# Performance work log

Measured on AMD Instinct MI355X. Metric: run time of the kernel, lower is better.

The kernel has to match this reference:

```python
import jax, jax.numpy as jnp
from jax import lax
import numpy as np

# GConv2d config (matches init_kwargs)
OUT_TRANSFORMS = 4  # rotations: 0, 90, 180, 270 degrees
STRIDE = 1
PADDING = 1


def setup_inputs() -> dict:
    key = jax.random.key(0)
    k1, k2, k3, k4 = jax.random.split(key, 4)
    B, IC_EFF, H, W = 16, 256, 64, 64   # IC_EFF = in_channels * in_transformations
    OC, K, F = 64, 4, 3                 # out_channels, num_dynamic_kernels, filter_size
    x = jax.random.normal(k1, (B, IC_EFF, H, W), dtype=jnp.float32)
    W_fc = jax.random.normal(k2, (K, IC_EFF), dtype=jnp.float32) * (1.0 / np.sqrt(IC_EFF))
    b_fc = jnp.zeros((K,), dtype=jnp.float32)
    kernel_bank = jax.random.normal(k3, (K, OC, IC_EFF, F, F), dtype=jnp.float32)
    return {"x": x, "W_fc": W_fc, "b_fc": b_fc, "kernel_bank": kernel_bank}


def reference(x, W_fc, b_fc, kernel_bank):
    B, C, H, W = x.shape
    # Dynamic routing: global average pool -> linear -> softmax over kernel bank
    pooled = x.mean(axis=(2, 3))                      # [B, C]
    coeffs = jax.nn.softmax(pooled @ W_fc.T + b_fc, axis=1)  # [B, K]
    # Sample-specific base kernels: mix of kernel bank
    base = jnp.einsum('bk,kocij->bocij', coeffs, kernel_bank)  # [B, oc, C, f, f]
    # P4 orientation expansion: rotate kernel spatially, stack along out-channels
    oriented = jnp.concatenate(
        [jnp.rot90(base, k, axes=(-2, -1)) for k in range(OUT_TRANSFORMS)], axis=1
    )  # [B, 4*oc, C, f, f]
    O, f = oriented.shape[1], oriented.shape[-1]
    # Batched per-sample conv via grouped convolution (one launch instead of B)
    xg = x.reshape(1, B * C, H, W)
    kg = oriented.reshape(B * O, C, f, f)
    out = lax.conv_general_dilated(
        xg, kg,
        window_strides=(STRIDE, STRIDE),
        padding=[(PADDING, PADDING), (PADDING, PADDING)],
        dimension_numbers=('NCHW', 'OIHW', 'NCHW'),
        feature_group_count=B,
    )  # [1, B*O, H', W']
    Ho, Wo = out.shape[-2], out.shape[-1]
    return out.reshape(B, O, Ho, Wo)
```

## Files before the change

kernel.cpp:

```cpp
#include <hip/hip_runtime.h>

#define B_  16
#define C_  256
#define O_  256

typedef short    bf16x8 __attribute__((ext_vector_type(8)));
typedef float    f32x16 __attribute__((ext_vector_type(16)));
typedef unsigned u32x4  __attribute__((ext_vector_type(4)));

#define XROW_SH  1056
#define XBC_SH   (66 * XROW_SH)
#define XT_BYTES ((size_t)B_ * 16 * XBC_SH * 2)

#define WTILE_SH 9216
#define WORP_BYTES ((size_t)B_ * 16 * 4 * WTILE_SH * 2)

#define XBUF_SH  10752

__device__ __forceinline__ unsigned cvtpk(float lo, float hi) {
    unsigned r;
    asm("v_cvt_pk_bf16_f32 %0, %1, %2" : "=v"(r) : "v"(lo), "v"(hi));
    return r;
}

__device__ __forceinline__ void gload16(const void* g, void* l) {
    __builtin_amdgcn_global_load_lds(
        (const __attribute__((address_space(1))) unsigned int*)g,
        (__attribute__((address_space(3))) unsigned int*)l, 16, 0, 0);
}

__global__ __launch_bounds__(256) void xprep_kernel(const float* __restrict__ x,
                                                    short* __restrict__ xT,
                                                    float* __restrict__ pooled4) {
    const int cg = blockIdx.x;
    const int b  = blockIdx.y;
    const int z  = blockIdx.z;
    const int t  = threadIdx.x;
    const int lane = t & 63, wv = t >> 6;
    const int cc = cg >> 1, lh = cg & 1;

    short* xTb = xT + (size_t)(b * 16 + cc) * XBC_SH;
    const float* xb = x + ((size_t)(b * C_ + cg * 8) << 12);

    {
        u32x4 zv = {0, 0, 0, 0};
        if (t < 32) {
            int r   = z * 16 + 1 + (t >> 1);
            int col = (t & 1) ? 65 : 0;
            *(u32x4*)&xTb[r * XROW_SH + lh * 528 + col * 8] = zv;
        }
        if (z == 0 || z == 3) {
            int row = (z == 0) ? 0 : 65;
            if (t < 66) *(u32x4*)&xTb[row * XROW_SH + lh * 528 + t * 8] = zv;
        }
    }

    float s[8] = {0.f, 0.f, 0.f, 0.f, 0.f, 0.f, 0.f, 0.f};
    const int px = lane;
#pragma unroll
    for (int r = 0; r < 4; ++r) {
        const int row = z * 16 + wv * 4 + r;
        const float* src = xb + row * 64 + px;
        float v[8];
#pragma unroll
        for (int i = 0; i < 8; ++i) { v[i] = src[(size_t)i << 12]; s[i] += v[i]; }
        u32x4 d = { cvtpk(v[0], v[1]), cvtpk(v[2], v[3]),
                    cvtpk(v[4], v[5]), cvtpk(v[6], v[7]) };
        *(u32x4*)&xTb[(row + 1) * XROW_SH + lh * 528 + (px + 1) * 8] = d;
    }

#pragma unroll
    for (int i = 0; i < 8; ++i)
#pragma unroll
        for (int off = 32; off; off >>= 1) s[i] += __shfl_xor(s[i], off, 64);

    __shared__ float pr[4][8];
    if (lane == 0) {
#pragma unroll
        for (int i = 0; i < 8; ++i) pr[wv][i] = s[i];
    }
    __syncthreads();
    if (t < 8) {
        float v = pr[0][t] + pr[1][t] + pr[2][t] + pr[3][t];
        pooled4[(z * B_ + b) * C_ + cg * 8 + t] = v * (1.0f / 4096.0f);
    }
}

__global__ __launch_bounds__(256) void mix_kernel(const float* __restrict__ bank,
                                                  const float* __restrict__ pooled4,
                                                  const float* __restrict__ W_fc,
                                                  const float* __restrict__ b_fc,
                                                  short* __restrict__ worp) {
    const int cc = blockIdx.x;
    const int og = blockIdx.y;
    const int t  = threadIdx.x;

    __shared__ float bankL[4][4][16][10];
    __shared__ float pl[64][4];
    __shared__ float cfs[16][4];

    for (int i = t; i < 2304; i += 256) {
        int k  = i / 576, r = i % 576;
        int oc = r / 144, r2 = r % 144;
        int c  = r2 / 9,  tap = r2 % 9;
        bankL[k][oc][c][tap] =
            bank[(((size_t)k * 64 + og * 4 + oc) * C_ + cc * 16 + c) * 9 + tap];
    }
    {
        int pair = t >> 2, seg = t & 3;
        int b = pair >> 2, k = pair & 3;
        float s = 0.f;
        for (int ci = 0; ci < 64; ++ci) {
            int c = seg * 64 + ci;
            float pv = pooled4[b * C_ + c] + pooled4[(B_ + b) * C_ + c]
                     + pooled4[(2 * B_ + b) * C_ + c] + pooled4[(3 * B_ + b) * C_ + c];
            s += pv * W_fc[k * C_ + c];
        }
        pl[pair][seg] = s;
    }
    __syncthreads();
    if (t < 64) {
        int b = t >> 2, k = t & 3;
        cfs[b][k] = pl[t][0] + pl[t][1] + pl[t][2] + pl[t][3] + b_fc[k];
    }
    __syncthreads();
    if (t < 16) {
        float l0 = cfs[t][0], l1 = cfs[t][1], l2 = cfs[t][2], l3 = cfs[t][3];
        float mx = fmaxf(fmaxf(l0, l1), fmaxf(l2, l3));
        float e0 = expf(l0 - mx), e1 = expf(l1 - mx);
        float e2 = expf(l2 - mx), e3 = expf(l3 - mx);
        float inv = 1.f / (e0 + e1 + e2 + e3);
        cfs[t][0] = e0 * inv; cfs[t][1] = e1 * inv;
        cfs[t][2] = e2 * inv; cfs[t][3] = e3 * inv;
    }
    __syncthreads();

    const int oc_l = t & 3;
    const int lhs  = (t >> 2) & 1;
    const int b    = (t >> 3) & 15;
    const int rep  = t >> 7;
    const int o64  = og * 4 + oc_l;

    const float c0 = cfs[b][0], c1 = cfs[b][1], c2 = cfs[b][2], c3 = cfs[b][3];
    float mixed[8][9];
#pragma unroll
    for (int ci = 0; ci < 8; ++ci)
#pragma unroll
        for (int tp = 0; tp < 9; ++tp)
            mixed[ci][tp] = c0 * bankL[0][oc_l][lhs * 8 + ci][tp]
                          + c1 * bankL[1][oc_l][lhs * 8 + ci][tp]
                          + c2 * bankL[2][oc_l][lhs * 8 + ci][tp]
                          + c3 * bankL[3][oc_l][lhs * 8 + ci][tp];

#define STOREOQ(OQ)                                                             \
    _Pragma("unroll")                                                           \
    for (int td = 0; td < 9; ++td) {                                            \
        const int ti = td / 3, tj = td % 3;                                     \
        int si, sj;                                                             \
        if      ((OQ) == 0) { si = ti;     sj = tj;     }                       \
        else if ((OQ) == 1) { si = tj;     sj = 2 - ti; }                       \
        else if ((OQ) == 2) { si = 2 - ti; sj = 2 - tj; }                       \
        else                { si = 2 - tj; sj = ti;     }                       \
        const int ts = si * 3 + sj;                                             \
        u32x4 d = { cvtpk(mixed[0][ts], mixed[1][ts]),                          \
                    cvtpk(mixed[2][ts], mixed[3][ts]),                          \
                    cvtpk(mixed[4][ts], mixed[5][ts]),                          \
                    cvtpk(mixed[6][ts], mixed[7][ts]) };                        \
        size_t base = ((((((size_t)b * 16 + cc) * 4 + (OQ)) * 9 + td) * 2       \
                        + lhs) * 64 + o64) * 8;                                 \
        *(u32x4*)&worp[base] = d;                                               \
    }

    if (rep == 0) { STOREOQ(0) STOREOQ(1) }
    else          { STOREOQ(2) STOREOQ(3) }
#undef STOREOQ
}

__global__ __launch_bounds__(256, 2)
void conv_mfma(const short* __restrict__ xT, const short* __restrict__ worp,
               float* __restrict__ out) {
    __shared__ short lds[2 * XBUF_SH + 2 * WTILE_SH];

    const int g    = blockIdx.x;
    const int w    = (g & 7) * 64 + (g >> 3);
    const int oq   = w & 3;
    const int m    = w >> 2;
    const int rowt = m & 7;
    const int b    = m >> 3;
    const int y0   = rowt * 8;

    const int t    = threadIdx.x;
    const int lane = t & 63;
    const int wid  = t >> 6;
    const int l31  = lane & 31;
    const int lh   = lane >> 5;

    const char* xsrcB = (const char*)xT
        + ((size_t)(b * 16) * XBC_SH + (size_t)y0 * XROW_SH) * 2 + lane * 16;
    const char* wsrcB = (const char*)worp
        + (((size_t)(b * 16) * 4) + oq) * (WTILE_SH * 2) + lane * 16;

#define STAGE(ccc, p)                                                           \
    { const char* xs = xsrcB + (size_t)(ccc) * (XBC_SH * 2);                    \
      const char* ws = wsrcB + (size_t)(ccc) * (4 * WTILE_SH * 2);              \
      char* xd = (char*)lds + (p) * (XBUF_SH * 2);                              \
      char* wd = (char*)lds + 2 * (XBUF_SH * 2) + (p) * (WTILE_SH * 2);         \
      for (int u = wid; u < 21; u += 4) gload16(xs + u * 1024, xd + u * 1024);  \
      for (int u = wid; u < 18; u += 4) gload16(ws + u * 1024, wd + u * 1024); }

#define BRD(r, s) (*(const bf16x8*)&xcur[(((r) * 2 + lh) * 66 + (s) + l31) * 8])
#define LOADROW(R, r)                                                           \
    { R[0] = BRD(r, 0);  R[1] = BRD(r, 1);  R[2] = BRD(r, 2);                   \
      R[3] = BRD(r, 32); R[4] = BRD(r, 33); R[5] = BRD(r, 34); }

#define TAPROW(i, RA, RB)                                                       \
    _Pragma("unroll")                                                           \
    for (int j = 0; j < 3; ++j) {                                               \
        const int tap = (i) * 3 + j;                                            \
        const short* wp = wcur + ((tap * 2 + lh) * 64 + l31) * 8;               \
        bf16x8 A0 = *(const bf16x8*)wp;                                         \
        bf16x8 A1 = *(const bf16x8*)(wp + 256);                                 \
        acc0[0] = __builtin_amdgcn_mfma_f32_32x32x16_bf16(A0, RA[j],     acc0[0], 0, 0, 0); \
        acc1[0] = __builtin_amdgcn_mfma_f32_32x32x16_bf16(A1, RA[j],     acc1[0], 0, 0, 0); \
        acc0[1] = __builtin_amdgcn_mfma_f32_32x32x16_bf16(A0, RA[3 + j], acc0[1], 0, 0, 0); \
        acc1[1] = __builtin_amdgcn_mfma_f32_32x32x16_bf16(A1, RA[3 + j], acc1[1], 0, 0, 0); \
        acc0[2] = __builtin_amdgcn_mfma_f32_32x32x16_bf16(A0, RB[j],     acc0[2], 0, 0, 0); \
        acc1[2] = __builtin_amdgcn_mfma_f32_32x32x16_bf16(A1, RB[j],     acc1[2], 0, 0, 0); \
        acc0[3] = __builtin_amdgcn_mfma_f32_32x32x16_bf16(A0, RB[3 + j], acc0[3], 0, 0, 0); \
        acc1[3] = __builtin_amdgcn_mfma_f32_32x32x16_bf16(A1, RB[3 + j], acc1[3], 0, 0, 0); \
    }

    f32x16 acc0[4] = {}, acc1[4] = {};

    STAGE(0, 0);
    __syncthreads();

    for (int cc = 0; cc < 16; ++cc) {
        const int p = cc & 1;
        if (cc < 15) STAGE(cc + 1, p ^ 1);
        const short* xcur = lds + p * XBUF_SH;
        const short* wcur = lds + 2 * XBUF_SH + p * WTILE_SH;

        bf16x8 R0[6], R1[6];
        __builtin_amdgcn_s_setprio(1);
        LOADROW(R0, 2 * wid);
        LOADROW(R1, 2 * wid + 1);
        TAPROW(0, R0, R1)
        LOADROW(R0, 2 * wid + 2)
        TAPROW(1, R1, R0)
        LOADROW(R1, 2 * wid + 3)
        TAPROW(2, R0, R1)
        __builtin_amdgcn_s_setprio(0);
        __syncthreads();
    }
#undef STAGE
#undef BRD
#undef LOADROW
#undef TAPROW

#pragma unroll
    for (int pf = 0; pf < 4; ++pf) {
        const int yb  = y0 + 2 * wid + (pf >> 1);
        const int xcb = 32 * (pf & 1) + l31;
#pragma unroll
        for (int r = 0; r < 16; ++r) {
            const int orow = (r & 3) + 8 * (r >> 2) + 4 * lh;
            const int o0   = oq * 64 + orow;
            __builtin_nontemporal_store(acc0[pf][r],
                &out[((size_t)(b * O_ + o0)      << 12) + yb * 64 + xcb]);
            __builtin_nontemporal_store(acc1[pf][r],
                &out[((size_t)(b * O_ + o0 + 32) << 12) + yb * 64 + xcb]);
        }
    }
}

extern "C" void kernel_launch(void* const* d_in, const int* in_sizes, int n_in,
                              void* d_out, int out_size, void* d_ws, size_t ws_size,
                              hipStream_t stream) {
    const float* x    = (const float*)d_in[0];
    const float* W_fc = (const float*)d_in[1];
    const float* b_fc = (const float*)d_in[2];
    const float* bank = (const float*)d_in[3];
    float* out = (float*)d_out;

    short* xTb     = (short*)d_ws;
    short* worp    = (short*)((char*)d_ws + XT_BYTES);
    float* pooled4 = (float*)((char*)d_ws + XT_BYTES + WORP_BYTES);

    xprep_kernel<<<dim3(32, 16, 4), 256, 0, stream>>>(x, xTb, pooled4);
    mix_kernel<<<dim3(16, 16), 256, 0, stream>>>(bank, pooled4, W_fc, b_fc, worp);
    conv_mfma<<<512, 256, 0, stream>>>(xTb, worp, out);
}
```

Measured before the change: 105.9 us.

## Vectorize xprep loads and split softmax coefficients into a single-block kernel

Result: slower. 109.2 us (+3.1%).

```diff
diff --git a/kernel.cpp b/kernel.cpp
--- a/kernel.cpp
+++ b/kernel.cpp
@@ -36,7 +36,7 @@
     const int b  = blockIdx.y;
     const int z  = blockIdx.z;
     const int t  = threadIdx.x;
-    const int lane = t & 63, wv = t >> 6;
+    const int wv = t >> 6;
     const int cc = cg >> 1, lh = cg & 1;
 
     short* xTb = xT + (size_t)(b * 16 + cc) * XBC_SH;
@@ -55,18 +55,24 @@
         }
     }
 
-    float s[8] = {0.f, 0.f, 0.f, 0.f, 0.f, 0.f, 0.f, 0.f};
-    const int px = lane;
-#pragma unroll
-    for (int r = 0; r < 4; ++r) {
-        const int row = z * 16 + wv * 4 + r;
-        const float* src = xb + row * 64 + px;
-        float v[8];
-#pragma unroll
-        for (int i = 0; i < 8; ++i) { v[i] = src[(size_t)i << 12]; s[i] += v[i]; }
-        u32x4 d = { cvtpk(v[0], v[1]), cvtpk(v[2], v[3]),
-                    cvtpk(v[4], v[5]), cvtpk(v[6], v[7]) };
-        *(u32x4*)&xTb[(row + 1) * XROW_SH + lh * 528 + (px + 1) * 8] = d;
+    const int q     = t & 15;
+    const int row16 = t >> 4;
+    const int row   = z * 16 + row16;
+
+    float v[8][4];
+    float s[8];
+#pragma unroll
+    for (int i = 0; i < 8; ++i) {
+        *(float4*)v[i] = *(const float4*)(xb + ((size_t)i << 12) + row * 64 + q * 4);
+        s[i] = v[i][0] + v[i][1] + v[i][2] + v[i][3];
+    }
+
+    short* dst = &xTb[(row + 1) * XROW_SH + lh * 528 + (q * 4 + 1) * 8];
+#pragma unroll
+    for (int p = 0; p < 4; ++p) {
+        u32x4 d = { cvtpk(v[0][p], v[1][p]), cvtpk(v[2][p], v[3][p]),
+                    cvtpk(v[4][p], v[5][p]), cvtpk(v[6][p], v[7][p]) };
+        *(u32x4*)(dst + p * 8) = d;
     }
 
 #pragma unroll
@@ -75,29 +81,59 @@
         for (int off = 32; off; off >>= 1) s[i] += __shfl_xor(s[i], off, 64);
 
     __shared__ float pr[4][8];
-    if (lane == 0) {
+    if ((t & 63) == 0) {
 #pragma unroll
         for (int i = 0; i < 8; ++i) pr[wv][i] = s[i];
     }
     __syncthreads();
     if (t < 8) {
-        float v = pr[0][t] + pr[1][t] + pr[2][t] + pr[3][t];
-        pooled4[(z * B_ + b) * C_ + cg * 8 + t] = v * (1.0f / 4096.0f);
+        float vv = pr[0][t] + pr[1][t] + pr[2][t] + pr[3][t];
+        pooled4[(z * B_ + b) * C_ + cg * 8 + t] = vv * (1.0f / 4096.0f);
+    }
+}
+
+__global__ __launch_bounds__(256) void coeff_kernel(const float* __restrict__ pooled4,
+                                                    const float* __restrict__ W_fc,
+                                                    const float* __restrict__ b_fc,
+                                                    float* __restrict__ cfs_g) {
+    __shared__ float pl[64][4];
+    const int t = threadIdx.x;
+    const int pair = t >> 2, seg = t & 3;
+    const int b = pair >> 2, k = pair & 3;
+    float s = 0.f;
+    for (int ci = 0; ci < 64; ++ci) {
+        int c = seg * 64 + ci;
+        float pv = pooled4[b * C_ + c] + pooled4[(B_ + b) * C_ + c]
+                 + pooled4[(2 * B_ + b) * C_ + c] + pooled4[(3 * B_ + b) * C_ + c];
+        s += pv * W_fc[k * C_ + c];
+    }
+    pl[pair][seg] = s;
+    __syncthreads();
+    if (t < 16) {
+        float l[4];
+#pragma unroll
+        for (int kk = 0; kk < 4; ++kk)
+            l[kk] = pl[t * 4 + kk][0] + pl[t * 4 + kk][1]
+                  + pl[t * 4 + kk][2] + pl[t * 4 + kk][3] + b_fc[kk];
+        float mx = fmaxf(fmaxf(l[0], l[1]), fmaxf(l[2], l[3]));
+        float e0 = expf(l[0] - mx), e1 = expf(l[1] - mx);
+        float e2 = expf(l[2] - mx), e3 = expf(l[3] - mx);
+        float inv = 1.f / (e0 + e1 + e2 + e3);
+        cfs_g[t * 4 + 0] = e0 * inv;
+        cfs_g[t * 4 + 1] = e1 * inv;
+        cfs_g[t * 4 + 2] = e2 * inv;
+        cfs_g[t * 4 + 3] = e3 * inv;
     }
 }
 
 __global__ __launch_bounds__(256) void mix_kernel(const float* __restrict__ bank,
-                                                  const float* __restrict__ pooled4,
-                                                  const float* __restrict__ W_fc,
-                                                  const float* __restrict__ b_fc,
+                                                  const float* __restrict__ cfs_g,
                                                   short* __restrict__ worp) {
     const int cc = blockIdx.x;
     const int og = blockIdx.y;
     const int t  = threadIdx.x;
 
     __shared__ float bankL[4][4][16][10];
-    __shared__ float pl[64][4];
-    __shared__ float cfs[16][4];
 
     for (int i = t; i < 2304; i += 256) {
         int k  = i / 576, r = i % 576;
@@ -106,33 +142,6 @@
         bankL[k][oc][c][tap] =
             bank[(((size_t)k * 64 + og * 4 + oc) * C_ + cc * 16 + c) * 9 + tap];
     }
-    {
-        int pair = t >> 2, seg = t & 3;
-        int b = pair >> 2, k = pair & 3;
-        float s = 0.f;
-        for (int ci = 0; ci < 64; ++ci) {
-            int c = seg * 64 + ci;
-            float pv = pooled4[b * C_ + c] + pooled4[(B_ + b) * C_ + c]
-                     + pooled4[(2 * B_ + b) * C_ + c] + pooled4[(3 * B_ + b) * C_ + c];
-            s += pv * W_fc[k * C_ + c];
-        }
-        pl[pair][seg] = s;
-    }
-    __syncthreads();
-    if (t < 64) {
-        int b = t >> 2, k = t & 3;
-        cfs[b][k] = pl[t][0] + pl[t][1] + pl[t][2] + pl[t][3] + b_fc[k];
-    }
-    __syncthreads();
-    if (t < 16) {
-        float l0 = cfs[t][0], l1 = cfs[t][1], l2 = cfs[t][2], l3 = cfs[t][3];
-        float mx = fmaxf(fmaxf(l0, l1), fmaxf(l2, l3));
-        float e0 = expf(l0 - mx), e1 = expf(l1 - mx);
-        float e2 = expf(l2 - mx), e3 = expf(l3 - mx);
-        float inv = 1.f / (e0 + e1 + e2 + e3);
-        cfs[t][0] = e0 * inv; cfs[t][1] = e1 * inv;
-        cfs[t][2] = e2 * inv; cfs[t][3] = e3 * inv;
-    }
     __syncthreads();
 
     const int oc_l = t & 3;
@@ -141,7 +150,8 @@
     const int rep  = t >> 7;
     const int o64  = og * 4 + oc_l;
 
-    const float c0 = cfs[b][0], c1 = cfs[b][1], c2 = cfs[b][2], c3 = cfs[b][3];
+    const float c0 = cfs_g[b * 4 + 0], c1 = cfs_g[b * 4 + 1];
+    const float c2 = cfs_g[b * 4 + 2], c3 = cfs_g[b * 4 + 3];
     float mixed[8][9];
 #pragma unroll
     for (int ci = 0; ci < 8; ++ci)
@@ -286,8 +296,10 @@
     short* xTb     = (short*)d_ws;
     short* worp    = (short*)((char*)d_ws + XT_BYTES);
     float* pooled4 = (float*)((char*)d_ws + XT_BYTES + WORP_BYTES);
+    float* cfs_g   = pooled4 + 4 * B_ * C_;
 
     xprep_kernel<<<dim3(32, 16, 4), 256, 0, stream>>>(x, xTb, pooled4);
-    mix_kernel<<<dim3(16, 16), 256, 0, stream>>>(bank, pooled4, W_fc, b_fc, worp);
+    coeff_kernel<<<1, 256, 0, stream>>>(pooled4, W_fc, b_fc, cfs_g);
+    mix_kernel<<<dim3(16, 16), 256, 0, stream>>>(bank, cfs_g, worp);
     conv_mfma<<<512, 256, 0, stream>>>(xTb, worp, out);
 }
```

## Double conv block to 512 threads covering two output quadrants with phased barriers

Applied to the files above, without the earlier changes.

After: 110.8 us. 1.05x slower.

```diff
diff --git a/kernel.cpp b/kernel.cpp
--- a/kernel.cpp
+++ b/kernel.cpp
@@ -16,6 +16,7 @@
 #define WORP_BYTES ((size_t)B_ * 16 * 4 * WTILE_SH * 2)
 
 #define XBUF_SH  10752
+#define WT2_SH   (2 * WTILE_SH)
 
 __device__ __forceinline__ unsigned cvtpk(float lo, float hi) {
     unsigned r;
@@ -81,8 +82,8 @@
     }
     __syncthreads();
     if (t < 8) {
-        float v = pr[0][t] + pr[1][t] + pr[2][t] + pr[3][t];
-        pooled4[(z * B_ + b) * C_ + cg * 8 + t] = v * (1.0f / 4096.0f);
+        float vv = pr[0][t] + pr[1][t] + pr[2][t] + pr[3][t];
+        pooled4[(z * B_ + b) * C_ + cg * 8 + t] = vv * (1.0f / 4096.0f);
     }
 }
 
@@ -176,37 +177,39 @@
 #undef STOREOQ
 }
 
-__global__ __launch_bounds__(256, 2)
+__global__ __launch_bounds__(512, 2)
 void conv_mfma(const short* __restrict__ xT, const short* __restrict__ worp,
                float* __restrict__ out) {
-    __shared__ short lds[2 * XBUF_SH + 2 * WTILE_SH];
+    __shared__ short lds[2 * XBUF_SH + 2 * WT2_SH];
 
     const int g    = blockIdx.x;
-    const int w    = (g & 7) * 64 + (g >> 3);
-    const int oq   = w & 3;
-    const int m    = w >> 2;
-    const int rowt = m & 7;
-    const int b    = m >> 3;
+    const int b_lo = g & 7;
+    const int r_   = g >> 3;
+    const int oh   = r_ & 1;
+    const int rowt = (r_ >> 1) & 7;
+    const int b    = ((r_ >> 4) << 3) | b_lo;
     const int y0   = rowt * 8;
 
     const int t    = threadIdx.x;
     const int lane = t & 63;
     const int wid  = t >> 6;
+    const int wm   = wid >> 2;
+    const int wn   = wid & 3;
     const int l31  = lane & 31;
     const int lh   = lane >> 5;
 
     const char* xsrcB = (const char*)xT
         + ((size_t)(b * 16) * XBC_SH + (size_t)y0 * XROW_SH) * 2 + lane * 16;
     const char* wsrcB = (const char*)worp
-        + (((size_t)(b * 16) * 4) + oq) * (WTILE_SH * 2) + lane * 16;
+        + ((size_t)(b * 16) * 4 + oh * 2) * (WTILE_SH * 2) + lane * 16;
 
 #define STAGE(ccc, p)                                                           \
     { const char* xs = xsrcB + (size_t)(ccc) * (XBC_SH * 2);                    \
       const char* ws = wsrcB + (size_t)(ccc) * (4 * WTILE_SH * 2);              \
       char* xd = (char*)lds + (p) * (XBUF_SH * 2);                              \
-      char* wd = (char*)lds + 2 * (XBUF_SH * 2) + (p) * (WTILE_SH * 2);         \
-      for (int u = wid; u < 21; u += 4) gload16(xs + u * 1024, xd + u * 1024);  \
-      for (int u = wid; u < 18; u += 4) gload16(ws + u * 1024, wd + u * 1024); }
+      char* wd = (char*)lds + 2 * (XBUF_SH * 2) + (p) * (WT2_SH * 2);           \
+      for (int u = wid; u < 21; u += 8) gload16(xs + u * 1024, xd + u * 1024);  \
+      for (int u = wid; u < 36; u += 8) gload16(ws + u * 1024, wd + u * 1024); }
 
 #define BRD(r, s) (*(const bf16x8*)&xcur[(((r) * 2 + lh) * 66 + (s) + l31) * 8])
 #define LOADROW(R, r)                                                           \
@@ -230,42 +233,60 @@
         acc1[3] = __builtin_amdgcn_mfma_f32_32x32x16_bf16(A1, RB[3 + j], acc1[3], 0, 0, 0); \
     }
 
+#define PHASE_BAR()                                                             \
+    __builtin_amdgcn_sched_barrier(0);                                          \
+    __builtin_amdgcn_s_barrier();                                               \
+    __builtin_amdgcn_sched_barrier(0);
+
     f32x16 acc0[4] = {}, acc1[4] = {};
 
     STAGE(0, 0);
-    __syncthreads();
+    asm volatile("s_waitcnt vmcnt(0)" ::: "memory");
+    PHASE_BAR();
 
     for (int cc = 0; cc < 16; ++cc) {
         const int p = cc & 1;
+        const short* xcur = lds + p * XBUF_SH;
+        const short* wcur = lds + 2 * XBUF_SH + p * WT2_SH + wm * WTILE_SH;
+
+        bf16x8 R0[6], R1[6];
+        LOADROW(R0, 2 * wn);
+        LOADROW(R1, 2 * wn + 1);
         if (cc < 15) STAGE(cc + 1, p ^ 1);
-        const short* xcur = lds + p * XBUF_SH;
-        const short* wcur = lds + 2 * XBUF_SH + p * WTILE_SH;
-
-        bf16x8 R0[6], R1[6];
+        PHASE_BAR();
         __builtin_amdgcn_s_setprio(1);
-        LOADROW(R0, 2 * wid);
-        LOADROW(R1, 2 * wid + 1);
         TAPROW(0, R0, R1)
-        LOADROW(R0, 2 * wid + 2)
+        __builtin_amdgcn_s_setprio(0);
+        PHASE_BAR();
+        LOADROW(R0, 2 * wn + 2);
+        PHASE_BAR();
+        __builtin_amdgcn_s_setprio(1);
         TAPROW(1, R1, R0)
-        LOADROW(R1, 2 * wid + 3)
+        __builtin_amdgcn_s_setprio(0);
+        PHASE_BAR();
+        LOADROW(R1, 2 * wn + 3);
+        PHASE_BAR();
+        __builtin_amdgcn_s_setprio(1);
         TAPROW(2, R0, R1)
         __builtin_amdgcn_s_setprio(0);
-        __syncthreads();
+        __builtin_amdgcn_sched_barrier(0);
+        asm volatile("s_waitcnt vmcnt(0)" ::: "memory");
+        PHASE_BAR();
     }
 #undef STAGE
 #undef BRD
 #undef LOADROW
 #undef TAPROW
+#undef PHASE_BAR
 
 #pragma unroll
     for (int pf = 0; pf < 4; ++pf) {
-        const int yb  = y0 + 2 * wid + (pf >> 1);
+        const int yb  = y0 + 2 * wn + (pf >> 1);
         const int xcb = 32 * (pf & 1) + l31;
 #pragma unroll
         for (int r = 0; r < 16; ++r) {
             const int orow = (r & 3) + 8 * (r >> 2) + 4 * lh;
-            const int o0   = oq * 64 + orow;
+            const int o0   = oh * 128 + wm * 64 + orow;
             __builtin_nontemporal_store(acc0[pf][r],
                 &out[((size_t)(b * O_ + o0)      << 12) + yb * 64 + xcb]);
             __builtin_nontemporal_store(acc1[pf][r],
@@ -289,5 +310,5 @@
 
     xprep_kernel<<<dim3(32, 16, 4), 256, 0, stream>>>(x, xTb, pooled4);
     mix_kernel<<<dim3(16, 16), 256, 0, stream>>>(bank, pooled4, W_fc, b_fc, worp);
-    conv_mfma<<<512, 256, 0, stream>>>(xTb, worp, out);
-}
+    conv_mfma<<<256, 512, 0, stream>>>(xTb, worp, out);
+}
```
